# Optimization experiments

Hardware: AMD Instinct MI355X
Metric: run time of the kernel (lower is better)

Reference implementation:

```python
import jax, jax.numpy as jnp
import numpy as np

NE, NR, D, B = 1_000_000, 1000, 32, 1_048_576
CURV = 1.0  # curvature K
HALF = D // 2


def _project(spatial):
    # recompute time component so point lies on hyperboloid <x,x>_L = -1/K
    x0 = jnp.sqrt(1.0 / CURV + jnp.sum(spatial * spatial, axis=-1, keepdims=True))
    return jnp.concatenate([x0, spatial], axis=-1)


def _lorentz_inner(u, v):
    return -u[..., 0] * v[..., 0] + jnp.sum(u[..., 1:] * v[..., 1:], axis=-1)


def setup_inputs() -> dict:
    key = jax.random.key(0)
    k0, k1, k2, k3, k4, k5, k6, k7 = jax.random.split(key, 8)
    tangent = jax.random.normal(k0, (NE, D), dtype=jnp.float32) * 0.01
    x0 = jnp.sqrt(1.0 / CURV + jnp.sum(tangent * tangent, axis=-1, keepdims=True))
    entity_emb = jnp.concatenate([x0, tangent], axis=-1)  # [NE, D+1]
    rel_boost_w = jax.random.normal(k1, (NR, D), dtype=jnp.float32) * 0.01
    rel_rot_w = jax.random.normal(k2, (NR, D), dtype=jnp.float32) * 0.01  # torch init is zeros; small noise for a nontrivial test
    rel_trans_w = jax.random.normal(k3, (NR, D), dtype=jnp.float32) * 0.01
    ent_bias_w = jax.random.normal(k4, (NE, 1), dtype=jnp.float32) * 0.01
    heads = jax.random.randint(k5, (B,), 0, NE)
    relations = jax.random.randint(k6, (B,), 0, NR)
    tails = jax.random.randint(k7, (B,), 0, NE)
    return {"heads": heads, "relations": relations, "tails": tails,
            "entity_emb": entity_emb, "rel_boost_w": rel_boost_w,
            "rel_rot_w": rel_rot_w, "rel_trans_w": rel_trans_w,
            "ent_bias_w": ent_bias_w}


def reference(heads, relations, tails, entity_emb, rel_boost_w, rel_rot_w, rel_trans_w, ent_bias_w):
    h = entity_emb[heads]                      # [B, D+1]
    t = entity_emb[tails]                      # [B, D+1]
    boost = rel_boost_w[relations]             # [B, D]
    rotation = rel_rot_w[relations]            # [B, D]
    translation = rel_trans_w[relations]       # [B, D]

    # --- spatial rotation: pairwise Givens rotations (i, i+HALF) ---
    x0 = h[..., 0:1]
    sp = h[..., 1:]
    a, b = sp[..., :HALF], sp[..., HALF:]
    c = jnp.cos(rotation[..., :HALF])
    s = jnp.sin(rotation[..., :HALF])
    rotated = jnp.concatenate([c * a - s * b, s * a + c * b], axis=-1)
    h_rot = jnp.concatenate([x0, rotated], axis=-1)

    # --- Lorentz boost along first spatial axis (only rapidity[..., 0] used) ---
    rap = jnp.clip(boost, -2.0, 2.0)
    c0 = jnp.cosh(rap[..., 0:1])
    s0 = jnp.sinh(rap[..., 0:1])
    bx0 = h_rot[..., 0:1]
    bx1 = h_rot[..., 1:2]
    new_x1 = bx0 * s0 + bx1 * c0
    new_spatial = jnp.concatenate([new_x1, h_rot[..., 2:]], axis=-1)
    h_boost = _project(new_spatial)  # time component recomputed by projection

    # --- exp map with tangent v = 0.1 * [0, translation] ---
    v = jnp.concatenate([jnp.zeros_like(translation[..., 0:1]), translation], axis=-1) * 0.1
    vn = jnp.sqrt(jnp.clip(_lorentz_inner(v, v), 1e-6, None))[..., None]
    res = jnp.cosh(vn) * h_boost + jnp.sinh(vn) * v / vn
    h_trans = _project(res[..., 1:])

    # --- Lorentz distance and score ---
    inner = _lorentz_inner(h_trans, t)
    ic = jnp.clip(-inner * CURV, 1.0 + 1e-6, None)
    dist = (1.0 / np.sqrt(CURV)) * jnp.arccosh(ic)
    b_h = ent_bias_w[heads][..., 0]
    b_t = ent_bias_w[tails][..., 0]
    return -dist * dist + b_h + b_t
```

## Files before the change

### kernel.cpp

```cpp
#include <hip/hip_runtime.h>
#include <hip/hip_fp16.h>
#include <math.h>

#define NR_ 1000
#define NE_ 1000000
#define D_ 32
#define HALF_ 16
#define EMB_DIM 33
#define H16_BYTES ((size_t)NE_ * 64)
#define T16_HALVES 64
#define T16_BYTES ((size_t)NR_ * T16_HALVES * 2)
#define HP_BYTES ((size_t)NR_ * 16)
#define ROWS_PER_BLOCK 64
#define FLOATS_PER_BLOCK (ROWS_PER_BLOCK * EMB_DIM)
#define REPACK_BLOCKS (NE_ / ROWS_PER_BLOCK)
#define TAB_BLOCKS 16

__global__ __launch_bounds__(256) void prep_kernel(
    const float* __restrict__ emb, const float* __restrict__ boost_w,
    const float* __restrict__ rot_w, const float* __restrict__ trans_w,
    unsigned int* __restrict__ h16, unsigned short* __restrict__ tab16,
    float4* __restrict__ hp_tab) {
  const int b = blockIdx.x;
  if (b < REPACK_BLOCKS) {
    __shared__ float s[FLOATS_PER_BLOCK];
    const int tid = threadIdx.x;
    const float* __restrict__ src = emb + (size_t)b * FLOATS_PER_BLOCK;
    #pragma unroll
    for (int k = 0; k < 8; ++k) s[tid + k * 256] = src[tid + k * 256];
    if (tid < FLOATS_PER_BLOCK - 2048) s[2048 + tid] = src[2048 + tid];
    __syncthreads();

    const int r = tid >> 2, q = tid & 3;
    const float* p = s + r * EMB_DIM + 1 + 4 * q;
    float a0 = p[0], a1 = p[1], a2 = p[2], a3 = p[3];
    float b0 = p[HALF_], b1 = p[HALF_ + 1], b2 = p[HALF_ + 2], b3 = p[HALF_ + 3];
    union { __half2 h; unsigned int u; } c0, c1, c2, c3;
    c0.h = __half2(__float2half_rn(a0), __float2half_rn(a1));
    c1.h = __half2(__float2half_rn(a2), __float2half_rn(a3));
    c2.h = __half2(__float2half_rn(b0), __float2half_rn(b1));
    c3.h = __half2(__float2half_rn(b2), __float2half_rn(b3));
    uint4 v = make_uint4(c0.u, c1.u, c2.u, c3.u);
    const size_t row = (size_t)b * ROWS_PER_BLOCK + r;
    *reinterpret_cast<uint4*>(h16 + row * 16 + 4 * q) = v;
    return;
  }
  const int t = (b - REPACK_BLOCKS) * 256 + threadIdx.x;
  const int r = t >> 2, q = t & 3;
  if (r >= NR_) return;
  const float* ro = rot_w   + (size_t)r * D_ + 4 * q;
  const float* ta = trans_w + (size_t)r * D_ + 4 * q;
  const float* tb = ta + HALF_;

  float ta0 = ta[0], ta1 = ta[1], ta2 = ta[2], ta3 = ta[3];
  float tb0 = tb[0], tb1 = tb[1], tb2 = tb[2], tb3 = tb[3];
  float s2 = ta0 * ta0;
  s2 = fmaf(ta1, ta1, s2); s2 = fmaf(ta2, ta2, s2); s2 = fmaf(ta3, ta3, s2);
  s2 = fmaf(tb0, tb0, s2); s2 = fmaf(tb1, tb1, s2);
  s2 = fmaf(tb2, tb2, s2); s2 = fmaf(tb3, tb3, s2);
  s2 += __shfl_xor(s2, 1);
  s2 += __shfl_xor(s2, 2);

  float vn = sqrtf(fmaxf(0.01f * s2, 1e-6f));
  float k  = sinhf(vn) / vn * 0.1f;

  const float cc0 = cosf(ro[0]), cc1 = cosf(ro[1]),
              cc2 = cosf(ro[2]), cc3 = cosf(ro[3]);
  const float ss0 = sinf(ro[0]), ss1 = sinf(ro[1]),
              ss2 = sinf(ro[2]), ss3 = sinf(ro[3]);

  union { __half2 h; unsigned int u; } p0, p1, p2, p3;
  p0.h = __half2(__float2half_rn(cc0), __float2half_rn(cc1));
  p1.h = __half2(__float2half_rn(cc2), __float2half_rn(cc3));
  p2.h = __half2(__float2half_rn(ss0), __float2half_rn(ss1));
  p3.h = __half2(__float2half_rn(ss2), __float2half_rn(ss3));
  *reinterpret_cast<uint4*>(tab16 + (size_t)r * T16_HALVES + 8 * q) =
      make_uint4(p0.u, p1.u, p2.u, p3.u);
  p0.h = __half2(__float2half_rn(k * ta0), __float2half_rn(k * ta1));
  p1.h = __half2(__float2half_rn(k * ta2), __float2half_rn(k * ta3));
  p2.h = __half2(__float2half_rn(k * tb0), __float2half_rn(k * tb1));
  p3.h = __half2(__float2half_rn(k * tb2), __float2half_rn(k * tb3));
  *reinterpret_cast<uint4*>(tab16 + (size_t)r * T16_HALVES + 32 + 8 * q) =
      make_uint4(p0.u, p1.u, p2.u, p3.u);

  if (q == 0) {
    float rap = fminf(fmaxf(boost_w[(size_t)r * D_], -2.f), 2.f);
    hp_tab[r] = make_float4(coshf(rap), sinhf(rap), coshf(vn), 0.f);
  }
}

__global__ __launch_bounds__(256) void lorentz_coop_kernel(
    const int* __restrict__ heads, const int* __restrict__ rels,
    const int* __restrict__ tails, const unsigned int* __restrict__ h16,
    const unsigned short* __restrict__ tab16, const float4* __restrict__ hp_tab,
    const float* __restrict__ bias, float* __restrict__ out, int n) {
  const int q = threadIdx.x & 3;
  const int e = (blockIdx.x * 256 + threadIdx.x) >> 2;
  const int i = (e < n) ? e : (n - 1);

  const int hd = heads[i];
  const int rl = rels[i];
  const int tl = tails[i];

  const uint4 hv = *reinterpret_cast<const uint4*>(h16 + (size_t)hd * 16 + 4 * q);
  const uint4 tv = *reinterpret_cast<const uint4*>(h16 + (size_t)tl * 16 + 4 * q);
  const uint4 rv = *reinterpret_cast<const uint4*>(
      tab16 + (size_t)rl * T16_HALVES + 8 * q);
  const uint4 kv = *reinterpret_cast<const uint4*>(
      tab16 + (size_t)rl * T16_HALVES + 32 + 8 * q);
  const float4 hp = hp_tab[rl];
  const float bsum = bias[hd] + bias[tl];

  union U2 { unsigned int u; __half2 h; };
  U2 rc0, rc1, rs0, rs1;
  rc0.u = rv.x; rc1.u = rv.y; rs0.u = rv.z; rs1.u = rv.w;
  const float2 c01 = __half22float2(rc0.h), c23 = __half22float2(rc1.h);
  const float2 s01 = __half22float2(rs0.h), s23 = __half22float2(rs1.h);
  U2 k0, k1, k2, k3;
  k0.u = kv.x; k1.u = kv.y; k2.u = kv.z; k3.u = kv.w;
  const float2 ka01 = __half22float2(k0.h), ka23 = __half22float2(k1.h);
  const float2 kb01 = __half22float2(k2.h), kb23 = __half22float2(k3.h);

  U2 u0, u1, u2, u3;
  u0.u = hv.x; u1.u = hv.y; u2.u = hv.z; u3.u = hv.w;
  const float2 fa01 = __half22float2(u0.h);
  const float2 fa23 = __half22float2(u1.h);
  const float2 fb01 = __half22float2(u2.h);
  const float2 fb23 = __half22float2(u3.h);
  const float a0 = fa01.x, a1 = fa01.y, a2 = fa23.x, a3 = fa23.y;
  const float b0 = fb01.x, b1 = fb01.y, b2 = fb23.x, b3 = fb23.y;

  float hsq = a0 * a0;
  hsq = fmaf(a1, a1, hsq); hsq = fmaf(a2, a2, hsq); hsq = fmaf(a3, a3, hsq);
  hsq = fmaf(b0, b0, hsq); hsq = fmaf(b1, b1, hsq);
  hsq = fmaf(b2, b2, hsq); hsq = fmaf(b3, b3, hsq);
  hsq += __shfl_xor(hsq, 1);
  hsq += __shfl_xor(hsq, 2);
  const float x0 = sqrtf(1.f + hsq);

  float rA0 = c01.x * a0 - s01.x * b0;
  float rA1 = c01.y * a1 - s01.y * b1;
  float rA2 = c23.x * a2 - s23.x * b2;
  float rA3 = c23.y * a3 - s23.y * b3;
  const float rB0 = fmaf(s01.x, a0, c01.x * b0);
  const float rB1 = fmaf(s01.y, a1, c01.y * b1);
  const float rB2 = fmaf(s23.x, a2, c23.x * b2);
  const float rB3 = fmaf(s23.y, a3, c23.y * b3);

  if (q == 0) rA0 = fmaf(x0, hp.y, rA0 * hp.x);
  const float cvn = hp.z;

  const float sA0 = fmaf(cvn, rA0, ka01.x);
  const float sA1 = fmaf(cvn, rA1, ka01.y);
  const float sA2 = fmaf(cvn, rA2, ka23.x);
  const float sA3 = fmaf(cvn, rA3, ka23.y);
  const float sB0 = fmaf(cvn, rB0, kb01.x);
  const float sB1 = fmaf(cvn, rB1, kb01.y);
  const float sB2 = fmaf(cvn, rB2, kb23.x);
  const float sB3 = fmaf(cvn, rB3, kb23.y);

  float n2 = sA0 * sA0;
  n2 = fmaf(sA1, sA1, n2); n2 = fmaf(sA2, sA2, n2); n2 = fmaf(sA3, sA3, n2);
  n2 = fmaf(sB0, sB0, n2); n2 = fmaf(sB1, sB1, n2);
  n2 = fmaf(sB2, sB2, n2); n2 = fmaf(sB3, sB3, n2);
  n2 += __shfl_xor(n2, 1);
  n2 += __shfl_xor(n2, 2);
  const float ht0 = sqrtf(1.f + n2);

  U2 w0, w1, w2, w3;
  w0.u = tv.x; w1.u = tv.y; w2.u = tv.z; w3.u = tv.w;
  const float2 ta01 = __half22float2(w0.h);
  const float2 ta23 = __half22float2(w1.h);
  const float2 tb01 = __half22float2(w2.h);
  const float2 tb23 = __half22float2(w3.h);

  float dot = sA0 * ta01.x;
  dot = fmaf(sA1, ta01.y, dot); dot = fmaf(sA2, ta23.x, dot);
  dot = fmaf(sA3, ta23.y, dot);
  dot = fmaf(sB0, tb01.x, dot); dot = fmaf(sB1, tb01.y, dot);
  dot = fmaf(sB2, tb23.x, dot); dot = fmaf(sB3, tb23.y, dot);

  float tsq = ta01.x * ta01.x;
  tsq = fmaf(ta01.y, ta01.y, tsq); tsq = fmaf(ta23.x, ta23.x, tsq);
  tsq = fmaf(ta23.y, ta23.y, tsq);
  tsq = fmaf(tb01.x, tb01.x, tsq); tsq = fmaf(tb01.y, tb01.y, tsq);
  tsq = fmaf(tb23.x, tb23.x, tsq); tsq = fmaf(tb23.y, tb23.y, tsq);

  dot += __shfl_xor(dot, 1);
  dot += __shfl_xor(dot, 2);
  tsq += __shfl_xor(tsq, 1);
  tsq += __shfl_xor(tsq, 2);
  const float t0 = sqrtf(1.f + tsq);

  const float neg_inner = fmaf(ht0, t0, -dot);
  const float ic = fmaxf(neg_inner, 1.0f + 1e-6f);
  const float dist = acoshf(ic);
  if (q == 0 && e < n) out[e] = bsum - dist * dist;
}

__global__ __launch_bounds__(256) void lorentz_fallback_kernel(
    const int* __restrict__ heads, const int* __restrict__ rels,
    const int* __restrict__ tails, const float* __restrict__ emb,
    const float* __restrict__ boost_w, const float* __restrict__ rot_w,
    const float* __restrict__ trans_w, const float* __restrict__ bias,
    float* __restrict__ out, int n) {
  int i = blockIdx.x * blockDim.x + threadIdx.x;
  if (i >= n) return;
  int hd = heads[i], rl = rels[i], tl = tails[i];
  const float* hrow = emb + (size_t)hd * EMB_DIM;
  const float* trow = emb + (size_t)tl * EMB_DIM;
  const float* ro = rot_w   + (size_t)rl * D_;
  const float* tr = trans_w + (size_t)rl * D_;
  float c[HALF_], s[HALF_], kt[D_];
  #pragma unroll
  for (int j = 0; j < HALF_; ++j) { float th = ro[j]; c[j] = cosf(th); s[j] = sinf(th); }
  float s2 = 0.f;
  #pragma unroll
  for (int j = 0; j < D_; ++j) { float v = tr[j]; s2 = fmaf(v, v, s2); }
  float vn = sqrtf(fmaxf(0.01f * s2, 1e-6f));
  float cvn = coshf(vn);
  float k = sinhf(vn) / vn * 0.1f;
  #pragma unroll
  for (int j = 0; j < D_; ++j) kt[j] = k * tr[j];
  float rap = fminf(fmaxf(boost_w[(size_t)rl * D_], -2.f), 2.f);
  float c0 = coshf(rap), s0 = sinhf(rap);
  float x0 = hrow[0];
  float r[D_];
  #pragma unroll
  for (int j = 0; j < HALF_; ++j) {
    float a = hrow[1 + j], b = hrow[1 + HALF_ + j];
    r[j] = c[j] * a - s[j] * b;
    r[HALF_ + j] = s[j] * a + c[j] * b;
  }
  r[0] = fmaf(x0, s0, r[0] * c0);
  float t0 = trow[0], n2 = 0.f, dot = 0.f;
  #pragma unroll
  for (int j = 0; j < D_; ++j) {
    float rsv = fmaf(cvn, r[j], kt[j]);
    n2  = fmaf(rsv, rsv, n2);
    dot = fmaf(rsv, trow[1 + j], dot);
  }
  float ht0 = sqrtf(1.f + n2);
  float neg_inner = fmaf(ht0, t0, -dot);
  float ic = fmaxf(neg_inner, 1.0f + 1e-6f);
  float dist = acoshf(ic);
  out[i] = bias[hd] + bias[tl] - dist * dist;
}

extern "C" void kernel_launch(void* const* d_in, const int* in_sizes, int n_in,
                              void* d_out, int out_size, void* d_ws, size_t ws_size,
                              hipStream_t stream) {
  const int*   heads  = (const int*)d_in[0];
  const int*   rels   = (const int*)d_in[1];
  const int*   tails  = (const int*)d_in[2];
  const float* emb    = (const float*)d_in[3];
  const float* boostw = (const float*)d_in[4];
  const float* rotw   = (const float*)d_in[5];
  const float* transw = (const float*)d_in[6];
  const float* bias   = (const float*)d_in[7];
  float* out = (float*)d_out;
  int n = in_sizes[0];

  dim3 block(256);

  if (ws_size >= H16_BYTES + T16_BYTES + HP_BYTES) {
    unsigned int* h16 = (unsigned int*)d_ws;
    unsigned short* tab16 = (unsigned short*)((char*)d_ws + H16_BYTES);
    float4* hp_tab = (float4*)((char*)d_ws + H16_BYTES + T16_BYTES);
    prep_kernel<<<dim3(REPACK_BLOCKS + TAB_BLOCKS), block, 0, stream>>>(
        emb, boostw, rotw, transw, h16, tab16, hp_tab);
    dim3 grid_main((n + 63) / 64);
    lorentz_coop_kernel<<<grid_main, block, 0, stream>>>(
        heads, rels, tails, h16, tab16, hp_tab, bias, out, n);
  } else {
    dim3 grid((n + 255) / 256);
    lorentz_fallback_kernel<<<grid, block, 0, stream>>>(
        heads, rels, tails, emb, boostw, rotw, transw, bias, out, n);
  }
}
```

Baseline: 272.0 us.

## Fuse prep and scoring into one persistent kernel with grid-wide barrier

Merges the fp16 repack/table-build kernel and the scoring kernel into a single persistent kernel of 2048 blocks that uses grid-stride loops. A global atomic arrival counter with spin-wait acts as a grid barrier between the two phases, and a tiny reset kernel clears the counter afterwards. This removes one kernel launch boundary and the tail drain between the two phases. In exchange, the repack drops its shared-memory staging and reads the 33-float rows directly. The barrier also depends on all 2048 blocks being co-resident; if they are not, it deadlocks until the clock timeout fires and then risks wrong results.

```diff
diff --git a/kernel.cpp b/kernel.cpp
--- a/kernel.cpp
+++ b/kernel.cpp
@@ -11,191 +11,203 @@
 #define T16_HALVES 64
 #define T16_BYTES ((size_t)NR_ * T16_HALVES * 2)
 #define HP_BYTES ((size_t)NR_ * 16)
-#define ROWS_PER_BLOCK 64
-#define FLOATS_PER_BLOCK (ROWS_PER_BLOCK * EMB_DIM)
-#define REPACK_BLOCKS (NE_ / ROWS_PER_BLOCK)
-#define TAB_BLOCKS 16
-
-__global__ __launch_bounds__(256) void prep_kernel(
-    const float* __restrict__ emb, const float* __restrict__ boost_w,
-    const float* __restrict__ rot_w, const float* __restrict__ trans_w,
+
+#define GRID_BLOCKS 2048
+#define REPACK_THREADS (NE_ * 4)
+#define TAB_THREADS (NR_ * 4)
+
+__device__ unsigned int g_arrive = 0;
+
+__global__ __launch_bounds__(256, 8) void fused_kernel(
+    const int* __restrict__ heads, const int* __restrict__ rels,
+    const int* __restrict__ tails, const float* __restrict__ emb,
+    const float* __restrict__ boost_w, const float* __restrict__ rot_w,
+    const float* __restrict__ trans_w, const float* __restrict__ bias,
     unsigned int* __restrict__ h16, unsigned short* __restrict__ tab16,
-    float4* __restrict__ hp_tab) {
-  const int b = blockIdx.x;
-  if (b < REPACK_BLOCKS) {
-    __shared__ float s[FLOATS_PER_BLOCK];
-    const int tid = threadIdx.x;
-    const float* __restrict__ src = emb + (size_t)b * FLOATS_PER_BLOCK;
-    #pragma unroll
-    for (int k = 0; k < 8; ++k) s[tid + k * 256] = src[tid + k * 256];
-    if (tid < FLOATS_PER_BLOCK - 2048) s[2048 + tid] = src[2048 + tid];
-    __syncthreads();
-
-    const int r = tid >> 2, q = tid & 3;
-    const float* p = s + r * EMB_DIM + 1 + 4 * q;
-    float a0 = p[0], a1 = p[1], a2 = p[2], a3 = p[3];
-    float b0 = p[HALF_], b1 = p[HALF_ + 1], b2 = p[HALF_ + 2], b3 = p[HALF_ + 3];
-    union { __half2 h; unsigned int u; } c0, c1, c2, c3;
-    c0.h = __half2(__float2half_rn(a0), __float2half_rn(a1));
-    c1.h = __half2(__float2half_rn(a2), __float2half_rn(a3));
-    c2.h = __half2(__float2half_rn(b0), __float2half_rn(b1));
-    c3.h = __half2(__float2half_rn(b2), __float2half_rn(b3));
-    uint4 v = make_uint4(c0.u, c1.u, c2.u, c3.u);
-    const size_t row = (size_t)b * ROWS_PER_BLOCK + r;
-    *reinterpret_cast<uint4*>(h16 + row * 16 + 4 * q) = v;
-    return;
-  }
-  const int t = (b - REPACK_BLOCKS) * 256 + threadIdx.x;
-  const int r = t >> 2, q = t & 3;
-  if (r >= NR_) return;
-  const float* ro = rot_w   + (size_t)r * D_ + 4 * q;
-  const float* ta = trans_w + (size_t)r * D_ + 4 * q;
-  const float* tb = ta + HALF_;
-
-  float ta0 = ta[0], ta1 = ta[1], ta2 = ta[2], ta3 = ta[3];
-  float tb0 = tb[0], tb1 = tb[1], tb2 = tb[2], tb3 = tb[3];
-  float s2 = ta0 * ta0;
-  s2 = fmaf(ta1, ta1, s2); s2 = fmaf(ta2, ta2, s2); s2 = fmaf(ta3, ta3, s2);
-  s2 = fmaf(tb0, tb0, s2); s2 = fmaf(tb1, tb1, s2);
-  s2 = fmaf(tb2, tb2, s2); s2 = fmaf(tb3, tb3, s2);
-  s2 += __shfl_xor(s2, 1);
-  s2 += __shfl_xor(s2, 2);
-
-  float vn = sqrtf(fmaxf(0.01f * s2, 1e-6f));
-  float k  = sinhf(vn) / vn * 0.1f;
-
-  const float cc0 = cosf(ro[0]), cc1 = cosf(ro[1]),
-              cc2 = cosf(ro[2]), cc3 = cosf(ro[3]);
-  const float ss0 = sinf(ro[0]), ss1 = sinf(ro[1]),
-              ss2 = sinf(ro[2]), ss3 = sinf(ro[3]);
-
-  union { __half2 h; unsigned int u; } p0, p1, p2, p3;
-  p0.h = __half2(__float2half_rn(cc0), __float2half_rn(cc1));
-  p1.h = __half2(__float2half_rn(cc2), __float2half_rn(cc3));
-  p2.h = __half2(__float2half_rn(ss0), __float2half_rn(ss1));
-  p3.h = __half2(__float2half_rn(ss2), __float2half_rn(ss3));
-  *reinterpret_cast<uint4*>(tab16 + (size_t)r * T16_HALVES + 8 * q) =
-      make_uint4(p0.u, p1.u, p2.u, p3.u);
-  p0.h = __half2(__float2half_rn(k * ta0), __float2half_rn(k * ta1));
-  p1.h = __half2(__float2half_rn(k * ta2), __float2half_rn(k * ta3));
-  p2.h = __half2(__float2half_rn(k * tb0), __float2half_rn(k * tb1));
-  p3.h = __half2(__float2half_rn(k * tb2), __float2half_rn(k * tb3));
-  *reinterpret_cast<uint4*>(tab16 + (size_t)r * T16_HALVES + 32 + 8 * q) =
-      make_uint4(p0.u, p1.u, p2.u, p3.u);
-
-  if (q == 0) {
-    float rap = fminf(fmaxf(boost_w[(size_t)r * D_], -2.f), 2.f);
-    hp_tab[r] = make_float4(coshf(rap), sinhf(rap), coshf(vn), 0.f);
-  }
-}
-
-__global__ __launch_bounds__(256) void lorentz_coop_kernel(
-    const int* __restrict__ heads, const int* __restrict__ rels,
-    const int* __restrict__ tails, const unsigned int* __restrict__ h16,
-    const unsigned short* __restrict__ tab16, const float4* __restrict__ hp_tab,
-    const float* __restrict__ bias, float* __restrict__ out, int n) {
-  const int q = threadIdx.x & 3;
-  const int e = (blockIdx.x * 256 + threadIdx.x) >> 2;
-  const int i = (e < n) ? e : (n - 1);
-
-  const int hd = heads[i];
-  const int rl = rels[i];
-  const int tl = tails[i];
-
-  const uint4 hv = *reinterpret_cast<const uint4*>(h16 + (size_t)hd * 16 + 4 * q);
-  const uint4 tv = *reinterpret_cast<const uint4*>(h16 + (size_t)tl * 16 + 4 * q);
-  const uint4 rv = *reinterpret_cast<const uint4*>(
-      tab16 + (size_t)rl * T16_HALVES + 8 * q);
-  const uint4 kv = *reinterpret_cast<const uint4*>(
-      tab16 + (size_t)rl * T16_HALVES + 32 + 8 * q);
-  const float4 hp = hp_tab[rl];
-  const float bsum = bias[hd] + bias[tl];
+    float4* __restrict__ hp_tab, float* __restrict__ out, int n) {
+  const int tid = threadIdx.x;
+  const long base0 = (long)blockIdx.x * 256 + tid;
+  const long gstride = (long)GRID_BLOCKS * 256;
 
   union U2 { unsigned int u; __half2 h; };
-  U2 rc0, rc1, rs0, rs1;
-  rc0.u = rv.x; rc1.u = rv.y; rs0.u = rv.z; rs1.u = rv.w;
-  const float2 c01 = __half22float2(rc0.h), c23 = __half22float2(rc1.h);
-  const float2 s01 = __half22float2(rs0.h), s23 = __half22float2(rs1.h);
-  U2 k0, k1, k2, k3;
-  k0.u = kv.x; k1.u = kv.y; k2.u = kv.z; k3.u = kv.w;
-  const float2 ka01 = __half22float2(k0.h), ka23 = __half22float2(k1.h);
-  const float2 kb01 = __half22float2(k2.h), kb23 = __half22float2(k3.h);
-
-  U2 u0, u1, u2, u3;
-  u0.u = hv.x; u1.u = hv.y; u2.u = hv.z; u3.u = hv.w;
-  const float2 fa01 = __half22float2(u0.h);
-  const float2 fa23 = __half22float2(u1.h);
-  const float2 fb01 = __half22float2(u2.h);
-  const float2 fb23 = __half22float2(u3.h);
-  const float a0 = fa01.x, a1 = fa01.y, a2 = fa23.x, a3 = fa23.y;
-  const float b0 = fb01.x, b1 = fb01.y, b2 = fb23.x, b3 = fb23.y;
-
-  float hsq = a0 * a0;
-  hsq = fmaf(a1, a1, hsq); hsq = fmaf(a2, a2, hsq); hsq = fmaf(a3, a3, hsq);
-  hsq = fmaf(b0, b0, hsq); hsq = fmaf(b1, b1, hsq);
-  hsq = fmaf(b2, b2, hsq); hsq = fmaf(b3, b3, hsq);
-  hsq += __shfl_xor(hsq, 1);
-  hsq += __shfl_xor(hsq, 2);
-  const float x0 = sqrtf(1.f + hsq);
-
-  float rA0 = c01.x * a0 - s01.x * b0;
-  float rA1 = c01.y * a1 - s01.y * b1;
-  float rA2 = c23.x * a2 - s23.x * b2;
-  float rA3 = c23.y * a3 - s23.y * b3;
-  const float rB0 = fmaf(s01.x, a0, c01.x * b0);
-  const float rB1 = fmaf(s01.y, a1, c01.y * b1);
-  const float rB2 = fmaf(s23.x, a2, c23.x * b2);
-  const float rB3 = fmaf(s23.y, a3, c23.y * b3);
-
-  if (q == 0) rA0 = fmaf(x0, hp.y, rA0 * hp.x);
-  const float cvn = hp.z;
-
-  const float sA0 = fmaf(cvn, rA0, ka01.x);
-  const float sA1 = fmaf(cvn, rA1, ka01.y);
-  const float sA2 = fmaf(cvn, rA2, ka23.x);
-  const float sA3 = fmaf(cvn, rA3, ka23.y);
-  const float sB0 = fmaf(cvn, rB0, kb01.x);
-  const float sB1 = fmaf(cvn, rB1, kb01.y);
-  const float sB2 = fmaf(cvn, rB2, kb23.x);
-  const float sB3 = fmaf(cvn, rB3, kb23.y);
-
-  float n2 = sA0 * sA0;
-  n2 = fmaf(sA1, sA1, n2); n2 = fmaf(sA2, sA2, n2); n2 = fmaf(sA3, sA3, n2);
-  n2 = fmaf(sB0, sB0, n2); n2 = fmaf(sB1, sB1, n2);
-  n2 = fmaf(sB2, sB2, n2); n2 = fmaf(sB3, sB3, n2);
-  n2 += __shfl_xor(n2, 1);
-  n2 += __shfl_xor(n2, 2);
-  const float ht0 = sqrtf(1.f + n2);
-
-  U2 w0, w1, w2, w3;
-  w0.u = tv.x; w1.u = tv.y; w2.u = tv.z; w3.u = tv.w;
-  const float2 ta01 = __half22float2(w0.h);
-  const float2 ta23 = __half22float2(w1.h);
-  const float2 tb01 = __half22float2(w2.h);
-  const float2 tb23 = __half22float2(w3.h);
-
-  float dot = sA0 * ta01.x;
-  dot = fmaf(sA1, ta01.y, dot); dot = fmaf(sA2, ta23.x, dot);
-  dot = fmaf(sA3, ta23.y, dot);
-  dot = fmaf(sB0, tb01.x, dot); dot = fmaf(sB1, tb01.y, dot);
-  dot = fmaf(sB2, tb23.x, dot); dot = fmaf(sB3, tb23.y, dot);
-
-  float tsq = ta01.x * ta01.x;
-  tsq = fmaf(ta01.y, ta01.y, tsq); tsq = fmaf(ta23.x, ta23.x, tsq);
-  tsq = fmaf(ta23.y, ta23.y, tsq);
-  tsq = fmaf(tb01.x, tb01.x, tsq); tsq = fmaf(tb01.y, tb01.y, tsq);
-  tsq = fmaf(tb23.x, tb23.x, tsq); tsq = fmaf(tb23.y, tb23.y, tsq);
-
-  dot += __shfl_xor(dot, 1);
-  dot += __shfl_xor(dot, 2);
-  tsq += __shfl_xor(tsq, 1);
-  tsq += __shfl_xor(tsq, 2);
-  const float t0 = sqrtf(1.f + tsq);
-
-  const float neg_inner = fmaf(ht0, t0, -dot);
-  const float ic = fmaxf(neg_inner, 1.0f + 1e-6f);
-  const float dist = acoshf(ic);
-  if (q == 0 && e < n) out[e] = bsum - dist * dist;
+
+  for (long t = base0; t < (long)REPACK_THREADS + TAB_THREADS; t += gstride) {
+    if (t < REPACK_THREADS) {
+      const int r = (int)(t >> 2), q = (int)(t & 3);
+      const float* p = emb + (size_t)r * EMB_DIM + 1 + 4 * q;
+      float a0 = p[0], a1 = p[1], a2 = p[2], a3 = p[3];
+      float b0 = p[HALF_], b1 = p[HALF_ + 1], b2 = p[HALF_ + 2], b3 = p[HALF_ + 3];
+      U2 c0, c1, c2, c3;
+      c0.h = __half2(__float2half_rn(a0), __float2half_rn(a1));
+      c1.h = __half2(__float2half_rn(a2), __float2half_rn(a3));
+      c2.h = __half2(__float2half_rn(b0), __float2half_rn(b1));
+      c3.h = __half2(__float2half_rn(b2), __float2half_rn(b3));
+      *reinterpret_cast<uint4*>(h16 + (size_t)r * 16 + 4 * q) =
+          make_uint4(c0.u, c1.u, c2.u, c3.u);
+    } else {
+      const int t2 = (int)(t - REPACK_THREADS);
+      const int r = t2 >> 2, q = t2 & 3;
+      const float* ro = rot_w   + (size_t)r * D_ + 4 * q;
+      const float* ta = trans_w + (size_t)r * D_ + 4 * q;
+      const float* tb = ta + HALF_;
+      float ta0 = ta[0], ta1 = ta[1], ta2 = ta[2], ta3 = ta[3];
+      float tb0 = tb[0], tb1 = tb[1], tb2 = tb[2], tb3 = tb[3];
+      float s2 = ta0 * ta0;
+      s2 = fmaf(ta1, ta1, s2); s2 = fmaf(ta2, ta2, s2); s2 = fmaf(ta3, ta3, s2);
+      s2 = fmaf(tb0, tb0, s2); s2 = fmaf(tb1, tb1, s2);
+      s2 = fmaf(tb2, tb2, s2); s2 = fmaf(tb3, tb3, s2);
+      s2 += __shfl_xor(s2, 1);
+      s2 += __shfl_xor(s2, 2);
+      float vn = sqrtf(fmaxf(0.01f * s2, 1e-6f));
+      float k  = sinhf(vn) / vn * 0.1f;
+      const float cc0 = cosf(ro[0]), cc1 = cosf(ro[1]),
+                  cc2 = cosf(ro[2]), cc3 = cosf(ro[3]);
+      const float ss0 = sinf(ro[0]), ss1 = sinf(ro[1]),
+                  ss2 = sinf(ro[2]), ss3 = sinf(ro[3]);
+      U2 p0, p1, p2, p3;
+      p0.h = __half2(__float2half_rn(cc0), __float2half_rn(cc1));
+      p1.h = __half2(__float2half_rn(cc2), __float2half_rn(cc3));
+      p2.h = __half2(__float2half_rn(ss0), __float2half_rn(ss1));
+      p3.h = __half2(__float2half_rn(ss2), __float2half_rn(ss3));
+      *reinterpret_cast<uint4*>(tab16 + (size_t)r * T16_HALVES + 8 * q) =
+          make_uint4(p0.u, p1.u, p2.u, p3.u);
+      p0.h = __half2(__float2half_rn(k * ta0), __float2half_rn(k * ta1));
+      p1.h = __half2(__float2half_rn(k * ta2), __float2half_rn(k * ta3));
+      p2.h = __half2(__float2half_rn(k * tb0), __float2half_rn(k * tb1));
+      p3.h = __half2(__float2half_rn(k * tb2), __float2half_rn(k * tb3));
+      *reinterpret_cast<uint4*>(tab16 + (size_t)r * T16_HALVES + 32 + 8 * q) =
+          make_uint4(p0.u, p1.u, p2.u, p3.u);
+      if (q == 0) {
+        float rap = fminf(fmaxf(boost_w[(size_t)r * D_], -2.f), 2.f);
+        hp_tab[r] = make_float4(coshf(rap), sinhf(rap), coshf(vn), 0.f);
+      }
+    }
+  }
+
+  __syncthreads();
+  if (tid == 0) {
+    __threadfence();
+    __hip_atomic_fetch_add(&g_arrive, 1u, __ATOMIC_RELEASE,
+                           __HIP_MEMORY_SCOPE_AGENT);
+    const long long tstart = (long long)clock64();
+    while (__hip_atomic_load(&g_arrive, __ATOMIC_ACQUIRE,
+                             __HIP_MEMORY_SCOPE_AGENT) < GRID_BLOCKS) {
+      __builtin_amdgcn_s_sleep(16);
+      if ((long long)clock64() - tstart > 2000000000LL) break;
+    }
+  }
+  __syncthreads();
+  __threadfence();
+
+  const long limit = (long)4 * n;
+  for (long gt = base0; gt < limit; gt += gstride) {
+    const int q = (int)(gt & 3);
+    const int e = (int)(gt >> 2);
+
+    const int hd = heads[e];
+    const int rl = rels[e];
+    const int tl = tails[e];
+
+    const uint4 hv = *reinterpret_cast<const uint4*>(h16 + (size_t)hd * 16 + 4 * q);
+    const uint4 tv = *reinterpret_cast<const uint4*>(h16 + (size_t)tl * 16 + 4 * q);
+    const uint4 rv = *reinterpret_cast<const uint4*>(
+        tab16 + (size_t)rl * T16_HALVES + 8 * q);
+    const uint4 kv = *reinterpret_cast<const uint4*>(
+        tab16 + (size_t)rl * T16_HALVES + 32 + 8 * q);
+    const float4 hp = hp_tab[rl];
+    const float bsum = bias[hd] + bias[tl];
+
+    U2 rc0, rc1, rs0, rs1;
+    rc0.u = rv.x; rc1.u = rv.y; rs0.u = rv.z; rs1.u = rv.w;
+    const float2 c01 = __half22float2(rc0.h), c23 = __half22float2(rc1.h);
+    const float2 s01 = __half22float2(rs0.h), s23 = __half22float2(rs1.h);
+    U2 k0, k1, k2, k3;
+    k0.u = kv.x; k1.u = kv.y; k2.u = kv.z; k3.u = kv.w;
+    const float2 ka01 = __half22float2(k0.h), ka23 = __half22float2(k1.h);
+    const float2 kb01 = __half22float2(k2.h), kb23 = __half22float2(k3.h);
+
+    U2 u0, u1, u2, u3;
+    u0.u = hv.x; u1.u = hv.y; u2.u = hv.z; u3.u = hv.w;
+    const float2 fa01 = __half22float2(u0.h);
+    const float2 fa23 = __half22float2(u1.h);
+    const float2 fb01 = __half22float2(u2.h);
+    const float2 fb23 = __half22float2(u3.h);
+    const float a0 = fa01.x, a1 = fa01.y, a2 = fa23.x, a3 = fa23.y;
+    const float b0 = fb01.x, b1 = fb01.y, b2 = fb23.x, b3 = fb23.y;
+
+    float hsq = a0 * a0;
+    hsq = fmaf(a1, a1, hsq); hsq = fmaf(a2, a2, hsq); hsq = fmaf(a3, a3, hsq);
+    hsq = fmaf(b0, b0, hsq); hsq = fmaf(b1, b1, hsq);
+    hsq = fmaf(b2, b2, hsq); hsq = fmaf(b3, b3, hsq);
+    hsq += __shfl_xor(hsq, 1);
+    hsq += __shfl_xor(hsq, 2);
+    const float x0 = sqrtf(1.f + hsq);
+
+    float rA0 = c01.x * a0 - s01.x * b0;
+    float rA1 = c01.y * a1 - s01.y * b1;
+    float rA2 = c23.x * a2 - s23.x * b2;
+    float rA3 = c23.y * a3 - s23.y * b3;
+    const float rB0 = fmaf(s01.x, a0, c01.x * b0);
+    const float rB1 = fmaf(s01.y, a1, c01.y * b1);
+    const float rB2 = fmaf(s23.x, a2, c23.x * b2);
+    const float rB3 = fmaf(s23.y, a3, c23.y * b3);
+
+    if (q == 0) rA0 = fmaf(x0, hp.y, rA0 * hp.x);
+    const float cvn = hp.z;
+
+    const float sA0 = fmaf(cvn, rA0, ka01.x);
+    const float sA1 = fmaf(cvn, rA1, ka01.y);
+    const float sA2 = fmaf(cvn, rA2, ka23.x);
+    const float sA3 = fmaf(cvn, rA3, ka23.y);
+    const float sB0 = fmaf(cvn, rB0, kb01.x);
+    const float sB1 = fmaf(cvn, rB1, kb01.y);
+    const float sB2 = fmaf(cvn, rB2, kb23.x);
+    const float sB3 = fmaf(cvn, rB3, kb23.y);
+
+    float n2 = sA0 * sA0;
+    n2 = fmaf(sA1, sA1, n2); n2 = fmaf(sA2, sA2, n2); n2 = fmaf(sA3, sA3, n2);
+    n2 = fmaf(sB0, sB0, n2); n2 = fmaf(sB1, sB1, n2);
+    n2 = fmaf(sB2, sB2, n2); n2 = fmaf(sB3, sB3, n2);
+    n2 += __shfl_xor(n2, 1);
+    n2 += __shfl_xor(n2, 2);
+    const float ht0 = sqrtf(1.f + n2);
+
+    U2 w0, w1, w2, w3;
+    w0.u = tv.x; w1.u = tv.y; w2.u = tv.z; w3.u = tv.w;
+    const float2 ta01 = __half22float2(w0.h);
+    const float2 ta23 = __half22float2(w1.h);
+    const float2 tb01 = __half22float2(w2.h);
+    const float2 tb23 = __half22float2(w3.h);
+
+    float dot = sA0 * ta01.x;
+    dot = fmaf(sA1, ta01.y, dot); dot = fmaf(sA2, ta23.x, dot);
+    dot = fmaf(sA3, ta23.y, dot);
+    dot = fmaf(sB0, tb01.x, dot); dot = fmaf(sB1, tb01.y, dot);
+    dot = fmaf(sB2, tb23.x, dot); dot = fmaf(sB3, tb23.y, dot);
+
+    float tsq = ta01.x * ta01.x;
+    tsq = fmaf(ta01.y, ta01.y, tsq); tsq = fmaf(ta23.x, ta23.x, tsq);
+    tsq = fmaf(ta23.y, ta23.y, tsq);
+    tsq = fmaf(tb01.x, tb01.x, tsq); tsq = fmaf(tb01.y, tb01.y, tsq);
+    tsq = fmaf(tb23.x, tb23.x, tsq); tsq = fmaf(tb23.y, tb23.y, tsq);
+
+    dot += __shfl_xor(dot, 1);
+    dot += __shfl_xor(dot, 2);
+    tsq += __shfl_xor(tsq, 1);
+    tsq += __shfl_xor(tsq, 2);
+    const float t0 = sqrtf(1.f + tsq);
+
+    const float neg_inner = fmaf(ht0, t0, -dot);
+    const float ic = fmaxf(neg_inner, 1.0f + 1e-6f);
+    const float dist = acoshf(ic);
+    if (q == 0) out[e] = bsum - dist * dist;
+  }
+}
+
+__global__ void reset_kernel() {
+  if (threadIdx.x == 0 && blockIdx.x == 0)
+    __hip_atomic_store(&g_arrive, 0u, __ATOMIC_RELAXED,
+                       __HIP_MEMORY_SCOPE_AGENT);
 }
 
 __global__ __launch_bounds__(256) void lorentz_fallback_kernel(
@@ -267,11 +279,10 @@
     unsigned int* h16 = (unsigned int*)d_ws;
     unsigned short* tab16 = (unsigned short*)((char*)d_ws + H16_BYTES);
     float4* hp_tab = (float4*)((char*)d_ws + H16_BYTES + T16_BYTES);
-    prep_kernel<<<dim3(REPACK_BLOCKS + TAB_BLOCKS), block, 0, stream>>>(
-        emb, boostw, rotw, transw, h16, tab16, hp_tab);
-    dim3 grid_main((n + 63) / 64);
-    lorentz_coop_kernel<<<grid_main, block, 0, stream>>>(
-        heads, rels, tails, h16, tab16, hp_tab, bias, out, n);
+    fused_kernel<<<dim3(GRID_BLOCKS), block, 0, stream>>>(
+        heads, rels, tails, emb, boostw, rotw, transw, bias,
+        h16, tab16, hp_tab, out, n);
+    reset_kernel<<<dim3(1), dim3(64), 0, stream>>>();
   } else {
     dim3 grid((n + 255) / 256);
     lorentz_fallback_kernel<<<grid, block, 0, stream>>>(
```

Result: slower. 832.3 us (+206.0%).
